# Kernel tuning notes

Measured on AMD Instinct MI355X. Metric: run time of the kernel, lower is better.

The kernel has to match this reference:

```python
import jax, jax.numpy as jnp
import numpy as np

H = 2048        # hidden_size
NH = 16         # num q heads
NKV = 4         # num kv heads
HD = 128        # head_dim
G = NH // NKV   # GQA group size
B = 32          # batch (decode sequences)
S = 4096        # max kv cache length per sequence
SCALE = HD ** -0.5
NEG = -1e30


def setup_inputs() -> dict:
    key = jax.random.key(0)
    ks = jax.random.split(key, 6)
    hidden_states = jax.random.normal(ks[0], (B, 1, H), dtype=jnp.float32)
    kv_cache = jax.random.normal(ks[1], (B, S, 2, NKV, HD), dtype=jnp.float32)
    seq_lens = jax.random.randint(ks[2], (B,), 1, S, dtype=jnp.int32)
    slot_mapping = seq_lens - 1  # write current token's k/v at its slot
    positions = (seq_lens - 1)[:, None].astype(jnp.int32)
    Wqkv = jax.random.normal(ks[3], (H, (NH + 2 * NKV) * HD), dtype=jnp.float32) * (H ** -0.5)
    bqkv = jax.random.normal(ks[4], ((NH + 2 * NKV) * HD,), dtype=jnp.float32) * 0.02
    Wo = jax.random.normal(ks[5], (NH * HD, H), dtype=jnp.float32) * ((NH * HD) ** -0.5)
    return {"hidden_states": hidden_states, "positions": positions, "kv_cache": kv_cache,
            "slot_mapping": slot_mapping, "seq_lens": seq_lens,
            "Wqkv": Wqkv, "bqkv": bqkv, "Wo": Wo}


def reference(hidden_states, positions, kv_cache, slot_mapping, seq_lens, Wqkv, bqkv, Wo):
    b, t, _ = hidden_states.shape  # t == 1 (decode)
    qkv = hidden_states.reshape(b * t, H) @ Wqkv + bqkv          # [B, (NH+2NKV)*HD]
    q, k, v = jnp.split(qkv, [NH * HD, (NH + NKV) * HD], axis=-1)
    q = q.reshape(b, NKV, G, HD)                                  # grouped-query layout
    k = k.reshape(b, NKV, HD)
    v = v.reshape(b, NKV, HD)
    # scatter current-step k/v into the paged cache at slot_mapping
    rows = jnp.arange(b)
    cache = kv_cache.at[rows, slot_mapping, 0].set(k)
    cache = cache.at[rows, slot_mapping, 1].set(v)
    keys = cache[:, :, 0]   # [B, S, NKV, HD]
    vals = cache[:, :, 1]   # [B, S, NKV, HD]
    # attention scores with ragged seq_lens mask
    scores = jnp.einsum('bkgd,bskd->bkgs', q, keys) * SCALE       # [B, NKV, G, S]
    valid = (jnp.arange(S)[None, :] < seq_lens[:, None])          # [B, S]
    scores = jnp.where(valid[:, None, None, :], scores, NEG)
    probs = jax.nn.softmax(scores, axis=-1)
    out = jnp.einsum('bkgs,bskd->bkgd', probs, vals)              # [B, NKV, G, HD]
    out = out.reshape(b * t, NH * HD)
    return (out @ Wo).reshape(b, t, H)
```

## Files before the change

### kernel.cpp

```cpp
#include <hip/hip_runtime.h>
#include <cstddef>

#define HQ 2048
#define NKVH 4
#define HDIM 128
#define QKV_N 3072
#define ATT_SCALE 0.08838834764831845f
#define KSPLIT 16
#define CHUNK 64
#define NCH 64

__device__ __forceinline__ float4 f4max(float4 a, float4 b) {
  return make_float4(fmaxf(a.x, b.x), fmaxf(a.y, b.y), fmaxf(a.z, b.z), fmaxf(a.w, b.w));
}

template <int N>
__global__ __launch_bounds__(256) void proj_kernel(const float* __restrict__ X,
                                                   const float* __restrict__ W,
                                                   float* __restrict__ part) {
  __shared__ union {
    float x[32][128];
    float red[32][4][64];
  } sm;
  const int t = threadIdx.x;
  const int c0 = blockIdx.x << 6;
  const int ksb = blockIdx.y;
  const int k0 = ksb << 7;
  const int c = t & 63;
  const int ksub = t >> 6;

#pragma unroll
  for (int i = 0; i < 4; ++i) {
    const int id = t + (i << 8);
    const int bb = id >> 5, kk = (id & 31) << 2;
    *reinterpret_cast<float4*>(&sm.x[bb][kk]) =
        *reinterpret_cast<const float4*>(X + bb * HQ + k0 + kk);
  }
  __syncthreads();

  float acc[32];
#pragma unroll
  for (int b = 0; b < 32; ++b) acc[b] = 0.f;

#pragma unroll
  for (int kk4 = 0; kk4 < 8; ++kk4) {
    const int kk = (ksub << 5) + (kk4 << 2);
    const float* wp = W + (size_t)(k0 + kk) * N + c0 + c;
    const float w0 = wp[0];
    const float w1 = wp[N];
    const float w2 = wp[2 * N];
    const float w3 = wp[3 * N];
#pragma unroll
    for (int b = 0; b < 32; ++b) {
      const float4 x4 = *reinterpret_cast<const float4*>(&sm.x[b][kk]);
      acc[b] = fmaf(x4.x, w0, acc[b]);
      acc[b] = fmaf(x4.y, w1, acc[b]);
      acc[b] = fmaf(x4.z, w2, acc[b]);
      acc[b] = fmaf(x4.w, w3, acc[b]);
    }
  }
  __syncthreads();
#pragma unroll
  for (int b = 0; b < 32; ++b) sm.red[b][ksub][c] = acc[b];
  __syncthreads();
#pragma unroll
  for (int i = 0; i < 8; ++i) {
    const int o = t + (i << 8);
    const int b = o >> 6, cc = o & 63;
    const float v = sm.red[b][0][cc] + sm.red[b][1][cc] + sm.red[b][2][cc] + sm.red[b][3][cc];
    part[(size_t)(ksb * 32 + b) * N + c0 + cc] = v;
  }
}

template <int NCOL, bool HAS_BIAS>
__global__ __launch_bounds__(256) void reduce_kernel(const float* __restrict__ part,
                                                     const float* __restrict__ bias,
                                                     float* __restrict__ out) {
  const int o = blockIdx.x * 256 + threadIdx.x;
  constexpr int total = 32 * NCOL;
  float s = 0.f;
#pragma unroll
  for (int ks = 0; ks < KSPLIT; ++ks) s += part[(size_t)ks * total + o];
  if (HAS_BIAS) s += bias[o % NCOL];
  out[o] = s;
}

__global__ __launch_bounds__(256, 4) void attn_kernel(const float* __restrict__ cache,
                                                      const int* __restrict__ seq_lens,
                                                      const int* __restrict__ slot_map,
                                                      const float* __restrict__ qkv,
                                                      float* __restrict__ ml,
                                                      float* __restrict__ accp) {
  __shared__ float pt[4][16][4];
  __shared__ float pvbuf[4][128][4];
  __shared__ float redm[4][4];
  __shared__ float redl[4][4];

  const int t = threadIdx.x;
  const int bid = blockIdx.x;
  const int chunk = bid & 63;
  const int kvh = (bid >> 6) & 3;
  const int b = bid >> 8;
  const int L = seq_lens[b];
  const int start = chunk << 6;
  if (start >= L) return;
  const int n = min(CHUNK, L - start);
  const int send = start + n;
  const int slot = slot_map[b];
  const float* __restrict__ qrow = qkv + b * QKV_N;
  const float* __restrict__ knew = qrow + 2048 + (kvh << 7);
  const float* __restrict__ vnew = qrow + 2560 + (kvh << 7);

  const int w = t >> 6, l = t & 63;
  const int l16 = l & 15, rq = l >> 4;
  const int wbase = w << 4;

  auto krow_ptr = [&](int r) -> const float* {
    int sg = start + r;
    sg = (sg < send) ? sg : start;
    return (sg == slot) ? knew : cache + (((size_t)((b << 12) + sg)) << 10) + (kvh << 7);
  };
  auto vrow_ptr = [&](int r) -> const float* {
    int sg = start + r;
    sg = (sg < send) ? sg : start;
    return (sg == slot) ? vnew : cache + (((size_t)((b << 12) + sg)) << 10) + 512 + (kvh << 7);
  };

  float4 qr[4][2];
#pragma unroll
  for (int g = 0; g < 4; ++g) {
#pragma unroll
    for (int e = 0; e < 2; ++e)
      qr[g][e] = *reinterpret_cast<const float4*>(qrow + ((kvh << 2) + g) * HDIM +
                                                  (l16 << 3) + (e << 2));
  }
  float4 ka[8];
#pragma unroll
  for (int rg = 0; rg < 4; ++rg) {
    const float* kp = krow_ptr(wbase + (rg << 2) + rq) + (l16 << 3);
    ka[2 * rg] = *reinterpret_cast<const float4*>(kp);
    ka[2 * rg + 1] = *reinterpret_cast<const float4*>(kp + 4);
  }
  float2 va[16];
#pragma unroll
  for (int s = 0; s < 16; ++s)
    va[s] = *reinterpret_cast<const float2*>(vrow_ptr(wbase + s) + (l << 1));

  float4 m4 = make_float4(-1e30f, -1e30f, -1e30f, -1e30f);
  float4 scr[4];
#pragma unroll
  for (int rg = 0; rg < 4; ++rg) {
    const float4 k0 = ka[2 * rg], k1 = ka[2 * rg + 1];
    float s0 = fmaf(k0.x, qr[0][0].x, fmaf(k0.y, qr[0][0].y, fmaf(k0.z, qr[0][0].z, k0.w * qr[0][0].w)));
    s0 = fmaf(k1.x, qr[0][1].x, fmaf(k1.y, qr[0][1].y, fmaf(k1.z, qr[0][1].z, fmaf(k1.w, qr[0][1].w, s0))));
    float s1 = fmaf(k0.x, qr[1][0].x, fmaf(k0.y, qr[1][0].y, fmaf(k0.z, qr[1][0].z, k0.w * qr[1][0].w)));
    s1 = fmaf(k1.x, qr[1][1].x, fmaf(k1.y, qr[1][1].y, fmaf(k1.z, qr[1][1].z, fmaf(k1.w, qr[1][1].w, s1))));
    float s2 = fmaf(k0.x, qr[2][0].x, fmaf(k0.y, qr[2][0].y, fmaf(k0.z, qr[2][0].z, k0.w * qr[2][0].w)));
    s2 = fmaf(k1.x, qr[2][1].x, fmaf(k1.y, qr[2][1].y, fmaf(k1.z, qr[2][1].z, fmaf(k1.w, qr[2][1].w, s2))));
    float s3 = fmaf(k0.x, qr[3][0].x, fmaf(k0.y, qr[3][0].y, fmaf(k0.z, qr[3][0].z, k0.w * qr[3][0].w)));
    s3 = fmaf(k1.x, qr[3][1].x, fmaf(k1.y, qr[3][1].y, fmaf(k1.z, qr[3][1].z, fmaf(k1.w, qr[3][1].w, s3))));
#pragma unroll
    for (int off = 1; off <= 8; off <<= 1) {
      s0 += __shfl_xor(s0, off);
      s1 += __shfl_xor(s1, off);
      s2 += __shfl_xor(s2, off);
      s3 += __shfl_xor(s3, off);
    }
    scr[rg] = make_float4(s0 * ATT_SCALE, s1 * ATT_SCALE, s2 * ATT_SCALE, s3 * ATT_SCALE);
    if (wbase + (rg << 2) + rq < n) m4 = f4max(m4, scr[rg]);
  }

  m4.x = fmaxf(m4.x, __shfl_xor(m4.x, 16));
  m4.y = fmaxf(m4.y, __shfl_xor(m4.y, 16));
  m4.z = fmaxf(m4.z, __shfl_xor(m4.z, 16));
  m4.w = fmaxf(m4.w, __shfl_xor(m4.w, 16));
  m4.x = fmaxf(m4.x, __shfl_xor(m4.x, 32));
  m4.y = fmaxf(m4.y, __shfl_xor(m4.y, 32));
  m4.z = fmaxf(m4.z, __shfl_xor(m4.z, 32));
  m4.w = fmaxf(m4.w, __shfl_xor(m4.w, 32));
  if (l == 0) *reinterpret_cast<float4*>(&redm[w][0]) = m4;
  __syncthreads();
  float4 M4 = *reinterpret_cast<const float4*>(&redm[0][0]);
  M4 = f4max(M4, *reinterpret_cast<const float4*>(&redm[1][0]));
  M4 = f4max(M4, *reinterpret_cast<const float4*>(&redm[2][0]));
  M4 = f4max(M4, *reinterpret_cast<const float4*>(&redm[3][0]));

  float4 lsum = make_float4(0.f, 0.f, 0.f, 0.f);
#pragma unroll
  for (int rg = 0; rg < 4; ++rg) {
    const int row = wbase + (rg << 2) + rq;
    float4 e = make_float4(0.f, 0.f, 0.f, 0.f);
    if (row < n) {
      e.x = __expf(scr[rg].x - M4.x);
      e.y = __expf(scr[rg].y - M4.y);
      e.z = __expf(scr[rg].z - M4.z);
      e.w = __expf(scr[rg].w - M4.w);
    }
    lsum.x += e.x; lsum.y += e.y; lsum.z += e.z; lsum.w += e.w;
    if (l16 == 0) *reinterpret_cast<float4*>(&pt[w][(rg << 2) + rq][0]) = e;
  }
  lsum.x += __shfl_xor(lsum.x, 16); lsum.y += __shfl_xor(lsum.y, 16);
  lsum.z += __shfl_xor(lsum.z, 16); lsum.w += __shfl_xor(lsum.w, 16);
  lsum.x += __shfl_xor(lsum.x, 32); lsum.y += __shfl_xor(lsum.y, 32);
  lsum.z += __shfl_xor(lsum.z, 32); lsum.w += __shfl_xor(lsum.w, 32);
  if (l == 0) *reinterpret_cast<float4*>(&redl[w][0]) = lsum;
  asm volatile("s_waitcnt lgkmcnt(0)" ::: "memory");

  float4 accA = make_float4(0.f, 0.f, 0.f, 0.f);
  float4 accB = make_float4(0.f, 0.f, 0.f, 0.f);
#pragma unroll
  for (int s = 0; s < 16; ++s) {
    const float4 p = *reinterpret_cast<const float4*>(&pt[w][s][0]);
    const float2 vv = va[s];
    accA.x = fmaf(p.x, vv.x, accA.x); accA.y = fmaf(p.y, vv.x, accA.y);
    accA.z = fmaf(p.z, vv.x, accA.z); accA.w = fmaf(p.w, vv.x, accA.w);
    accB.x = fmaf(p.x, vv.y, accB.x); accB.y = fmaf(p.y, vv.y, accB.y);
    accB.z = fmaf(p.z, vv.y, accB.z); accB.w = fmaf(p.w, vv.y, accB.w);
  }

  *reinterpret_cast<float4*>(&pvbuf[w][l << 1][0]) = accA;
  *reinterpret_cast<float4*>(&pvbuf[w][(l << 1) + 1][0]) = accB;
  __syncthreads();

  if (t < 128) {
    const int d = t;
    float4 s0 = *reinterpret_cast<const float4*>(&pvbuf[0][d][0]);
    const float4 s1 = *reinterpret_cast<const float4*>(&pvbuf[1][d][0]);
    const float4 s2 = *reinterpret_cast<const float4*>(&pvbuf[2][d][0]);
    const float4 s3 = *reinterpret_cast<const float4*>(&pvbuf[3][d][0]);
    s0.x += s1.x + s2.x + s3.x;
    s0.y += s1.y + s2.y + s3.y;
    s0.z += s1.z + s2.z + s3.z;
    s0.w += s1.w + s2.w + s3.w;
    float* ap = accp + (size_t)bid * 512;
    ap[d] = s0.x;
    ap[128 + d] = s0.y;
    ap[256 + d] = s0.z;
    ap[384 + d] = s0.w;
  }
  if (t == 0) {
    float4 Lt = *reinterpret_cast<const float4*>(&redl[0][0]);
    const float4 l1 = *reinterpret_cast<const float4*>(&redl[1][0]);
    const float4 l2 = *reinterpret_cast<const float4*>(&redl[2][0]);
    const float4 l3 = *reinterpret_cast<const float4*>(&redl[3][0]);
    Lt.x += l1.x + l2.x + l3.x;
    Lt.y += l1.y + l2.y + l3.y;
    Lt.z += l1.z + l2.z + l3.z;
    Lt.w += l1.w + l2.w + l3.w;
    *reinterpret_cast<float4*>(ml + (size_t)bid * 8) = M4;
    *reinterpret_cast<float4*>(ml + (size_t)bid * 8 + 4) = Lt;
  }
}

__global__ __launch_bounds__(128) void combine_kernel(const int* __restrict__ seq_lens,
                                                      const float* __restrict__ ml,
                                                      const float* __restrict__ accp,
                                                      float* __restrict__ attn) {
  const int blk = blockIdx.x;
  const int g = blk & 3, kvh = (blk >> 2) & 3, b = blk >> 4;
  const int d = threadIdx.x;
  const int L = seq_lens[b];
  const int nch = (L + CHUNK - 1) >> 6;
  const int base = (b * 4 + kvh) * NCH;

  float M = -1e30f;
  for (int c = 0; c < nch; ++c) M = fmaxf(M, ml[(size_t)(base + c) * 8 + g]);
  float osum = 0.f, lsum = 0.f;
  for (int c = 0; c < nch; ++c) {
    const int idx = base + c;
    const float mc = ml[(size_t)idx * 8 + g];
    const float lc = ml[(size_t)idx * 8 + 4 + g];
    const float wgt = __expf(mc - M);
    lsum = fmaf(lc, wgt, lsum);
    osum = fmaf(wgt, accp[(size_t)idx * 512 + g * 128 + d], osum);
  }
  attn[(size_t)b * HQ + kvh * 512 + g * 128 + d] = osum / lsum;
}

extern "C" void kernel_launch(void* const* d_in, const int* in_sizes, int n_in,
                              void* d_out, int out_size, void* d_ws, size_t ws_size,
                              hipStream_t stream) {
  const float* hidden = (const float*)d_in[0];
  const float* cache = (const float*)d_in[2];
  const int* slot_map = (const int*)d_in[3];
  const int* seq_lens = (const int*)d_in[4];
  const float* Wqkv = (const float*)d_in[5];
  const float* bqkv = (const float*)d_in[6];
  const float* Wo = (const float*)d_in[7];
  float* out = (float*)d_out;
  float* ws = (float*)d_ws;

  float* qkv_part = ws;
  float* qkv      = ws + 1572864;
  float* ml       = ws + 1671168;
  float* accp     = ws + 1736704;
  float* attn     = ws + 5931008;
  float* o_part   = ws + 5996544;

  proj_kernel<QKV_N><<<dim3(48, KSPLIT), 256, 0, stream>>>(hidden, Wqkv, qkv_part);
  reduce_kernel<QKV_N, true><<<384, 256, 0, stream>>>(qkv_part, bqkv, qkv);
  attn_kernel<<<8192, 256, 0, stream>>>(cache, seq_lens, slot_map, qkv, ml, accp);
  combine_kernel<<<512, 128, 0, stream>>>(seq_lens, ml, accp, attn);
  proj_kernel<HQ><<<dim3(32, KSPLIT), 256, 0, stream>>>(attn, Wo, o_part);
  reduce_kernel<HQ, false><<<256, 256, 0, stream>>>(o_part, nullptr, out);
}
```

Baseline: 132.6 us.

## Reorder attention grid chunk-major and issue K/V loads via inline asm with staged waits

The block index now maps kv-head and batch to the fastest-varying bits and chunk to the slowest, so early-terminating blocks for short sequences are spread across the grid instead of clustered. Partial outputs are written to a separately computed slot so the combine kernel layout is unchanged. Q/K loads use a strided split (lane*4 and +64) and all Q/K/V loads are issued as raw global_load asm with explicit vmcnt waits, so V loads stay in flight during the QK and softmax phase. Occupancy hint drops from 4 to 3 blocks per SIMD to give the compiler more registers. The hand-written waitcnt counts depend on the exact number and order of loads issued.

```diff
diff --git a/kernel.cpp b/kernel.cpp
--- a/kernel.cpp
+++ b/kernel.cpp
@@ -9,6 +9,9 @@
 #define KSPLIT 16
 #define CHUNK 64
 #define NCH 64
+
+#define GLOAD4(dst, p) asm volatile("global_load_dwordx4 %0, %1, off" : "=v"(dst) : "v"(p))
+#define GLOAD2(dst, p) asm volatile("global_load_dwordx2 %0, %1, off" : "=v"(dst) : "v"(p))
 
 __device__ __forceinline__ float4 f4max(float4 a, float4 b) {
   return make_float4(fmaxf(a.x, b.x), fmaxf(a.y, b.y), fmaxf(a.z, b.z), fmaxf(a.w, b.w));
@@ -85,7 +88,7 @@
   out[o] = s;
 }
 
-__global__ __launch_bounds__(256, 4) void attn_kernel(const float* __restrict__ cache,
+__global__ __launch_bounds__(256, 3) void attn_kernel(const float* __restrict__ cache,
                                                       const int* __restrict__ seq_lens,
                                                       const int* __restrict__ slot_map,
                                                       const float* __restrict__ qkv,
@@ -98,9 +101,9 @@
 
   const int t = threadIdx.x;
   const int bid = blockIdx.x;
-  const int chunk = bid & 63;
-  const int kvh = (bid >> 6) & 3;
-  const int b = bid >> 8;
+  const int kvh = bid & 3;
+  const int b = (bid >> 2) & 31;
+  const int chunk = bid >> 7;
   const int L = seq_lens[b];
   const int start = chunk << 6;
   if (start >= L) return;
@@ -110,6 +113,7 @@
   const float* __restrict__ qrow = qkv + b * QKV_N;
   const float* __restrict__ knew = qrow + 2048 + (kvh << 7);
   const float* __restrict__ vnew = qrow + 2560 + (kvh << 7);
+  const int oslot = (((b << 2) | kvh) << 6) + chunk;
 
   const int w = t >> 6, l = t & 63;
   const int l16 = l & 15, rq = l >> 4;
@@ -129,22 +133,24 @@
   float4 qr[4][2];
 #pragma unroll
   for (int g = 0; g < 4; ++g) {
-#pragma unroll
-    for (int e = 0; e < 2; ++e)
-      qr[g][e] = *reinterpret_cast<const float4*>(qrow + ((kvh << 2) + g) * HDIM +
-                                                  (l16 << 3) + (e << 2));
+    const float* qp = qrow + ((kvh << 2) + g) * HDIM + (l16 << 2);
+    GLOAD4(qr[g][0], qp);
+    GLOAD4(qr[g][1], qp + 64);
   }
   float4 ka[8];
 #pragma unroll
   for (int rg = 0; rg < 4; ++rg) {
-    const float* kp = krow_ptr(wbase + (rg << 2) + rq) + (l16 << 3);
-    ka[2 * rg] = *reinterpret_cast<const float4*>(kp);
-    ka[2 * rg + 1] = *reinterpret_cast<const float4*>(kp + 4);
+    const float* kp = krow_ptr(wbase + (rg << 2) + rq) + (l16 << 2);
+    GLOAD4(ka[2 * rg], kp);
+    GLOAD4(ka[2 * rg + 1], kp + 64);
   }
   float2 va[16];
 #pragma unroll
-  for (int s = 0; s < 16; ++s)
-    va[s] = *reinterpret_cast<const float2*>(vrow_ptr(wbase + s) + (l << 1));
+  for (int s = 0; s < 16; ++s) {
+    GLOAD2(va[s], vrow_ptr(wbase + s) + (l << 1));
+  }
+  asm volatile("s_waitcnt vmcnt(16)" ::: "memory");
+  __builtin_amdgcn_sched_barrier(0);
 
   float4 m4 = make_float4(-1e30f, -1e30f, -1e30f, -1e30f);
   float4 scr[4];
@@ -206,6 +212,9 @@
   if (l == 0) *reinterpret_cast<float4*>(&redl[w][0]) = lsum;
   asm volatile("s_waitcnt lgkmcnt(0)" ::: "memory");
 
+  asm volatile("s_waitcnt vmcnt(0)" ::: "memory");
+  __builtin_amdgcn_sched_barrier(0);
+
   float4 accA = make_float4(0.f, 0.f, 0.f, 0.f);
   float4 accB = make_float4(0.f, 0.f, 0.f, 0.f);
 #pragma unroll
@@ -232,7 +241,7 @@
     s0.y += s1.y + s2.y + s3.y;
     s0.z += s1.z + s2.z + s3.z;
     s0.w += s1.w + s2.w + s3.w;
-    float* ap = accp + (size_t)bid * 512;
+    float* ap = accp + (size_t)oslot * 512;
     ap[d] = s0.x;
     ap[128 + d] = s0.y;
     ap[256 + d] = s0.z;
@@ -247,8 +256,8 @@
     Lt.y += l1.y + l2.y + l3.y;
     Lt.z += l1.z + l2.z + l3.z;
     Lt.w += l1.w + l2.w + l3.w;
-    *reinterpret_cast<float4*>(ml + (size_t)bid * 8) = M4;
-    *reinterpret_cast<float4*>(ml + (size_t)bid * 8 + 4) = Lt;
+    *reinterpret_cast<float4*>(ml + (size_t)oslot * 8) = M4;
+    *reinterpret_cast<float4*>(ml + (size_t)oslot * 8 + 4) = Lt;
   }
 }
 
```

Measured after the change: 137.8 us. 1.04x slower.
